# Kernel tuning notes

Hardware: AMD Instinct MI355X
Metric: run time of the kernel (lower is better)

The kernel has to match this reference:

```python
import jax, jax.numpy as jnp
import numpy as np
import math

EMB = 2048
HEADS = 16
HEAD_DIM = EMB // HEADS  # 128
SCALE = math.sqrt(HEAD_DIM)


def srms_norm(x, eps_min=1e-12):
    # Scaled RMS norm over last dim, computed in float32.
    d = x.shape[-1]
    xf = x.astype(jnp.float32)
    norm = jnp.linalg.norm(xf * (1.0 / math.sqrt(d)), axis=-1, keepdims=True)
    norm = jnp.maximum(norm, eps_min)
    return (xf / norm).astype(x.dtype)


def setup_inputs() -> dict:
    key = jax.random.key(0)
    ks = jax.random.split(key, 6)
    x = jax.random.normal(ks[0], (4, 4096, EMB), dtype=jnp.float32)
    # xavier-normal std for square D x D: sqrt(2/(D+D)) = 1/sqrt(D); gain=1 (lth=None)
    std = 1.0 / math.sqrt(EMB)
    Wq = jax.random.normal(ks[1], (EMB, EMB), dtype=jnp.float32) * std
    Wk = jax.random.normal(ks[2], (EMB, EMB), dtype=jnp.float32) * std
    Wv = jax.random.normal(ks[3], (EMB, EMB), dtype=jnp.float32) * std
    Wu = jax.random.normal(ks[4], (EMB, EMB), dtype=jnp.float32) * std
    Wo = jax.random.normal(ks[5], (EMB, EMB), dtype=jnp.float32) * std
    return {"x": x, "Wq": Wq, "Wk": Wk, "Wv": Wv, "Wu": Wu, "Wo": Wo}


def reference(x, Wq, Wk, Wv, Wu, Wo):
    B, L, D = x.shape
    H, dh = HEADS, HEAD_DIM
    # projections (weights stored as [in, out])
    q = (x @ Wq).reshape(B, L, H, dh).transpose(0, 2, 1, 3)  # [B,H,L,dh]
    k = (x @ Wk).reshape(B, L, H, dh).transpose(0, 2, 1, 3)
    v = (x @ Wv).reshape(B, L, H, dh).transpose(0, 2, 1, 3)
    u = (x @ Wu).reshape(B, L, H, dh).transpose(0, 2, 1, 3)
    q = jax.nn.relu(q) / SCALE
    k = jax.nn.relu(k) / SCALE
    u = jax.nn.silu(u)
    # linear retention: kv state [B,H,dh,dh], then q @ kv
    kv = jnp.einsum('bhlk,bhlv->bhkv', k, v)
    out = jnp.einsum('bhlk,bhkv->bhlv', q, kv)
    out = srms_norm(out) * u
    out = out.transpose(0, 2, 1, 3).reshape(B, L, D)
    return out @ Wo
```

## Files before the change

### kernel.cpp

```cpp
#include <hip/hip_runtime.h>
#include <hip/hip_bf16.h>
#include <cstdint>


typedef __attribute__((ext_vector_type(8))) short short8;
typedef __attribute__((ext_vector_type(4))) float f32x4;

#define DEVI static __device__ __forceinline__

DEVI float bf2f(unsigned short u) {
    union { unsigned int i; float f; } w; w.i = ((unsigned int)u) << 16; return w.f;
}
DEVI unsigned short f2bf(float f) {
    union { float f; unsigned int i; } w; w.f = f;
    return (unsigned short)((w.i + 0x7fffu + ((w.i >> 16) & 1u)) >> 16);
}

#define GLDS16(gp, lp) __builtin_amdgcn_global_load_lds( \
    (const __attribute__((address_space(1))) void*)(gp), \
    (__attribute__((address_space(3))) void*)(lp), 16, 0, 0)

__global__ void probe_dtype(const unsigned short* __restrict__ x, int* flag) {
    __shared__ int cnt;
    if (threadIdx.x == 0) cnt = 0;
    __syncthreads();
    int c = 0;
    for (int i = threadIdx.x; i < 4096; i += 256) {
        float a = fabsf(bf2f(x[i]));
        if (!(a <= 1e4f) || (a != 0.0f && a < 1e-4f)) ++c;
    }
    atomicAdd(&cnt, c);
    __syncthreads();
    if (threadIdx.x == 0) *flag = (cnt < 512) ? 1 : 0;
}

__global__ void wconvert(const void* __restrict__ Wq, const void* __restrict__ Wk,
                         const void* __restrict__ Wv, const void* __restrict__ Wu,
                         const void* __restrict__ Wo,
                         unsigned short* __restrict__ wt4,
                         unsigned short* __restrict__ wot,
                         const int* __restrict__ flag) {
    const int z = blockIdx.z;
    const void* W = (z == 0) ? Wq : (z == 1) ? Wk : (z == 2) ? Wv : (z == 3) ? Wu : Wo;
    const bool isbf = (*flag != 0);
    __shared__ float tile[32][33];
    const int j0 = blockIdx.x * 32, i0 = blockIdx.y * 32;
    const int tx = threadIdx.x, ty = threadIdx.y;
#pragma unroll
    for (int r = 0; r < 4; ++r) {
        const int i = i0 + ty * 4 + r;
        float v;
        if (isbf) v = bf2f(((const unsigned short*)W)[i * 2048 + j0 + tx]);
        else      v = ((const float*)W)[i * 2048 + j0 + tx];
        tile[ty * 4 + r][tx] = v;
    }
    __syncthreads();
#pragma unroll
    for (int r = 0; r < 4; ++r) {
        const int j = j0 + ty * 4 + r;
        const unsigned short bv = f2bf(tile[tx][ty * 4 + r]);
        if (z < 4) wt4[(long)(z * 2048 + j) * 2048 + i0 + tx] = bv;
        else       wot[(long)j * 2048 + i0 + tx] = bv;
    }
}

__global__ void xconvert(const void* __restrict__ X, unsigned short* __restrict__ xb,
                         const int* __restrict__ flag) {
    const bool isbf = (*flag != 0);
    const long i = (long)blockIdx.x * 256 + threadIdx.x;
    if (isbf) {
        ((uint4*)xb)[i] = ((const uint4*)X)[i];
    } else {
        const float4 f0 = ((const float4*)X)[2 * i];
        const float4 f1 = ((const float4*)X)[2 * i + 1];
        union { unsigned short us[8]; uint4 v; } o;
        o.us[0] = f2bf(f0.x); o.us[1] = f2bf(f0.y); o.us[2] = f2bf(f0.z); o.us[3] = f2bf(f0.w);
        o.us[4] = f2bf(f1.x); o.us[5] = f2bf(f1.y); o.us[6] = f2bf(f1.z); o.us[7] = f2bf(f1.w);
        ((uint4*)xb)[i] = o.v;
    }
}

DEVI void gemm_core(const unsigned short* __restrict__ Ag,
                    const unsigned short* __restrict__ Bg,
                    unsigned short* As, unsigned short* Bs,
                    f32x4 acc[8][4], const int tid) {
    const int wave = tid >> 6, lane = tid & 63;
    const int wr = wave >> 2, wc = wave & 3;
    const int srow = tid >> 2;
    const int lsl = (tid & 3) ^ ((srow >> 1) & 3);
    const unsigned short* ga0 = Ag + (long)srow * 2048 + lsl * 8;
    const unsigned short* ga1 = ga0 + 128 * 2048;
    const unsigned short* gb0 = Bg + (long)srow * 2048 + lsl * 8;
    const unsigned short* gb1 = gb0 + 128 * 2048;
    const int ldsb = wave * 512;

    const int psl = ((lane >> 4) ^ (((lane & 15) >> 1) & 3)) * 8;
    const int abase = (wr * 128 + (lane & 15)) * 32 + psl;
    const int bbase = (wc * 64 + (lane & 15)) * 32 + psl;

#define ISSUE(tt) do { \
    const int _b = (tt) & 3; const int _ko = (tt) * 32; \
    GLDS16(ga0 + _ko, As + _b * 8192 + ldsb); \
    GLDS16(ga1 + _ko, As + _b * 8192 + 4096 + ldsb); \
    GLDS16(gb0 + _ko, Bs + _b * 8192 + ldsb); \
    GLDS16(gb1 + _ko, Bs + _b * 8192 + 4096 + ldsb); \
} while (0)

    ISSUE(0); ISSUE(1); ISSUE(2);
    for (int t = 0; t < 64; ++t) {
        asm volatile("s_waitcnt vmcnt(8)" ::: "memory");
        asm volatile("s_barrier" ::: "memory");
        int tt = t + 3; if (tt >= 64) tt -= 64;
        ISSUE(tt);
        const unsigned short* a_ = As + (t & 3) * 8192;
        const unsigned short* b_ = Bs + (t & 3) * 8192;
        short8 af[8], bf[4];
#pragma unroll
        for (int fm = 0; fm < 8; ++fm) af[fm] = *(const short8*)(a_ + abase + fm * 512);
#pragma unroll
        for (int fn = 0; fn < 4; ++fn) bf[fn] = *(const short8*)(b_ + bbase + fn * 512);
        __builtin_amdgcn_s_setprio(1);
#pragma unroll
        for (int fm = 0; fm < 8; ++fm)
#pragma unroll
            for (int fn = 0; fn < 4; ++fn)
                acc[fm][fn] = __builtin_amdgcn_mfma_f32_16x16x32_bf16(af[fm], bf[fn], acc[fm][fn], 0, 0, 0);
        __builtin_amdgcn_s_setprio(0);
        asm volatile("s_barrier" ::: "memory");
    }
    asm volatile("s_waitcnt vmcnt(0)" ::: "memory");
#undef ISSUE
}

__global__ __launch_bounds__(512, 2)
void gemm_qkvu(const unsigned short* __restrict__ Xb,
               const unsigned short* __restrict__ Wt4,
               unsigned short* __restrict__ Qb, unsigned short* __restrict__ Kb,
               unsigned short* __restrict__ Vb, unsigned short* __restrict__ Ub) {
    __shared__ unsigned short As[4 * 8192];
    __shared__ unsigned short Bs[4 * 8192];
    const int orig = blockIdx.x;
    const int flat = (orig & 7) * 256 + (orig >> 3);
    const int mt = flat & 63, nt = flat >> 6;
    const long m0 = (long)mt * 256;
    const int tid = threadIdx.x;
    f32x4 acc[8][4] = {};

    gemm_core(Xb + m0 * 2048, Wt4 + (long)nt * 256 * 2048, As, Bs, acc, tid);

    const int wave = tid >> 6, lane = tid & 63;
    const int wr = wave >> 2, wc = wave & 3;
    const int seg = nt >> 3;
    unsigned short* outp = (seg == 0) ? Qb : (seg == 1) ? Kb : (seg == 2) ? Vb : Ub;
    const int cl0 = (nt & 7) * 256 + wc * 64;
#pragma unroll
    for (int fm = 0; fm < 8; ++fm) {
#pragma unroll
        for (int fn = 0; fn < 4; ++fn) {
            const int col = cl0 + fn * 16 + (lane & 15);
#pragma unroll
            for (int r = 0; r < 4; ++r) {
                const long row = m0 + wr * 128 + fm * 16 + ((lane >> 4) << 2) + r;
                float v = acc[fm][fn][r];
                if (seg <= 1)      v = fmaxf(v, 0.0f) * 0.08838834764831845f;
                else if (seg == 3) v = v / (1.0f + __expf(-v));
                outp[row * 2048 + col] = f2bf(v);
            }
        }
    }
}

__global__ __launch_bounds__(512, 2)
void gemm_out(const unsigned short* __restrict__ Obuf,
              const unsigned short* __restrict__ Wot,
              void* __restrict__ out, const int* __restrict__ flag) {
    __shared__ unsigned short As[4 * 8192];
    __shared__ unsigned short Bs[4 * 8192];
    const int orig = blockIdx.x;
    const int flat = (orig & 7) * 64 + (orig >> 3);
    const int mt = flat & 63, nt = flat >> 6;
    const long m0 = (long)mt * 256;
    const int j0 = nt * 256;
    const int tid = threadIdx.x;
    f32x4 acc[8][4] = {};

    gemm_core(Obuf + m0 * 2048, Wot + (long)j0 * 2048, As, Bs, acc, tid);

    const int wave = tid >> 6, lane = tid & 63;
    const int wr = wave >> 2, wc = wave & 3;
    const bool isbf = (*flag != 0);
#pragma unroll
    for (int fm = 0; fm < 8; ++fm) {
#pragma unroll
        for (int fn = 0; fn < 4; ++fn) {
            const int col = j0 + wc * 64 + fn * 16 + (lane & 15);
#pragma unroll
            for (int r = 0; r < 4; ++r) {
                const long row = m0 + wr * 128 + fm * 16 + ((lane >> 4) << 2) + r;
                const float v = acc[fm][fn][r];
                if (isbf) ((unsigned short*)out)[row * 2048 + col] = f2bf(v);
                else      ((float*)out)[row * 2048 + col] = v;
            }
        }
    }
}

__global__ void kv_accum(const unsigned short* __restrict__ Kb,
                         const unsigned short* __restrict__ Vb,
                         float* __restrict__ KVpart) {
    __shared__ unsigned short Kt[128 * 64];
    __shared__ unsigned short Vt[128 * 64];
    const int bh = blockIdx.x;
    const int chunk = blockIdx.y;
    const int b = bh >> 4, h = bh & 15;
    const int t = threadIdx.x, wave = t >> 6, lane = t & 63;
    const int wr = wave >> 1, wc = wave & 1;
    const int l0 = (t & 15) * 4;
    const int dkg = t >> 4;
    const long gbase = ((long)b * 4096 + chunk * 1024) * 2048 + h * 128;
    f32x4 acc[4][4] = {};

    for (int tile = 0; tile < 16; ++tile) {
        __syncthreads();
        short8 kr[4], vr[4];
#pragma unroll
        for (int li = 0; li < 4; ++li) {
            const long go = gbase + (long)(tile * 64 + l0 + li) * 2048 + dkg * 8;
            kr[li] = *(const short8*)(Kb + go);
            vr[li] = *(const short8*)(Vb + go);
        }
#pragma unroll
        for (int i = 0; i < 8; ++i) {
            const int row = dkg * 8 + i;
            const int lin = row * 128 + l0 * 2;
            const int off = (lin ^ ((row & 7) << 4)) >> 1;
            union { unsigned short us[4]; unsigned long long u; } pk, pv;
#pragma unroll
            for (int li = 0; li < 4; ++li) { pk.us[li] = (unsigned short)kr[li][i]; pv.us[li] = (unsigned short)vr[li][i]; }
            *(unsigned long long*)(Kt + off) = pk.u;
            *(unsigned long long*)(Vt + off) = pv.u;
        }
        __syncthreads();
#pragma unroll
        for (int ks = 0; ks < 2; ++ks) {
            const int kof = ks * 64 + (lane >> 4) * 16;
            short8 a[4], bfr[4];
#pragma unroll
            for (int f = 0; f < 4; ++f) {
                const int ra = wr * 64 + f * 16 + (lane & 15);
                const int rb = wc * 64 + f * 16 + (lane & 15);
                a[f]   = *(const short8*)(Vt + (((ra * 128 + kof) ^ ((ra & 7) << 4)) >> 1));
                bfr[f] = *(const short8*)(Kt + (((rb * 128 + kof) ^ ((rb & 7) << 4)) >> 1));
            }
#pragma unroll
            for (int fm = 0; fm < 4; ++fm)
#pragma unroll
                for (int fn = 0; fn < 4; ++fn)
                    acc[fm][fn] = __builtin_amdgcn_mfma_f32_16x16x32_bf16(a[fm], bfr[fn], acc[fm][fn], 0, 0, 0);
        }
    }
    float* dst = KVpart + ((long)chunk * 64 + bh) * 16384;
#pragma unroll
    for (int fm = 0; fm < 4; ++fm)
#pragma unroll
        for (int fn = 0; fn < 4; ++fn)
#pragma unroll
            for (int r = 0; r < 4; ++r) {
                const int dv = wr * 64 + fm * 16 + ((lane >> 4) << 2) + r;
                const int dk = wc * 64 + fn * 16 + (lane & 15);
                dst[dv * 128 + dk] = acc[fm][fn][r];
            }
}

__global__ void kv_finalize(const float* __restrict__ KVpart,
                            unsigned short* __restrict__ KVhi,
                            unsigned short* __restrict__ KVlo) {
    const long base = ((long)blockIdx.x * 256 + threadIdx.x) * 4;
    float4 s0 = *(const float4*)(KVpart + base);
    const float4 s1 = *(const float4*)(KVpart + 1048576 + base);
    const float4 s2 = *(const float4*)(KVpart + 2097152 + base);
    const float4 s3 = *(const float4*)(KVpart + 3145728 + base);
    float s[4] = { s0.x + s1.x + s2.x + s3.x, s0.y + s1.y + s2.y + s3.y,
                   s0.z + s1.z + s2.z + s3.z, s0.w + s1.w + s2.w + s3.w };
    union { unsigned short us[4]; unsigned long long u; } hi, lo;
#pragma unroll
    for (int j = 0; j < 4; ++j) {
        hi.us[j] = f2bf(s[j]);
        lo.us[j] = f2bf(s[j] - bf2f(hi.us[j]));
    }
    *(unsigned long long*)(KVhi + base) = hi.u;
    *(unsigned long long*)(KVlo + base) = lo.u;
}

__global__ void o_norm(const unsigned short* __restrict__ Qb,
                       const unsigned short* __restrict__ Ub,
                       const unsigned short* __restrict__ KVhi,
                       const unsigned short* __restrict__ KVlo,
                       unsigned short* __restrict__ Ob) {
    __shared__ unsigned short Qs[128 * 128];
    const int tid = threadIdx.x, wave = tid >> 6, lane = tid & 63;
    const int tile = blockIdx.x;
    const int bh = blockIdx.y;
    const int b = bh >> 4, h = bh & 15;
    const long n0 = (long)b * 4096 + tile * 128;

    const int qrow = tid >> 4;
    const int qcol = (tid & 15) * 8;
#pragma unroll
    for (int i = 0; i < 8; ++i)
        GLDS16(Qb + (n0 + i * 16 + qrow) * 2048 + h * 128 + qcol, Qs + i * 2048 + wave * 512);
    __syncthreads();

    const unsigned short* KH = KVhi + (long)bh * 16384;
    const unsigned short* KL = KVlo + (long)bh * 16384;
    f32x4 acc[2][8] = {};
#pragma unroll
    for (int kk = 0; kk < 4; ++kk) {
        const short8 a0 = *(const short8*)(Qs + (wave * 32 + (lane & 15)) * 128 + kk * 32 + (lane >> 4) * 8);
        const short8 a1 = *(const short8*)(Qs + (wave * 32 + 16 + (lane & 15)) * 128 + kk * 32 + (lane >> 4) * 8);
#pragma unroll
        for (int fn = 0; fn < 8; ++fn) {
            const int bo = (fn * 16 + (lane & 15)) * 128 + kk * 32 + (lane >> 4) * 8;
            const short8 bhi = *(const short8*)(KH + bo);
            const short8 blo = *(const short8*)(KL + bo);
            acc[0][fn] = __builtin_amdgcn_mfma_f32_16x16x32_bf16(a0, bhi, acc[0][fn], 0, 0, 0);
            acc[0][fn] = __builtin_amdgcn_mfma_f32_16x16x32_bf16(a0, blo, acc[0][fn], 0, 0, 0);
            acc[1][fn] = __builtin_amdgcn_mfma_f32_16x16x32_bf16(a1, bhi, acc[1][fn], 0, 0, 0);
            acc[1][fn] = __builtin_amdgcn_mfma_f32_16x16x32_bf16(a1, blo, acc[1][fn], 0, 0, 0);
        }
    }

#pragma unroll
    for (int fm = 0; fm < 2; ++fm) {
#pragma unroll
        for (int r = 0; r < 4; ++r) {
            float ssq = 0.0f;
#pragma unroll
            for (int fn = 0; fn < 8; ++fn) { const float v = acc[fm][fn][r]; ssq += v * v; }
            ssq += __shfl_xor(ssq, 1);
            ssq += __shfl_xor(ssq, 2);
            ssq += __shfl_xor(ssq, 4);
            ssq += __shfl_xor(ssq, 8);
            const float nrm = fmaxf(sqrtf(ssq) * 0.08838834764831845f, 1e-12f);
            const float scl = 1.0f / nrm;
            const long row = n0 + wave * 32 + fm * 16 + ((lane >> 4) << 2) + r;
#pragma unroll
            for (int fn = 0; fn < 8; ++fn) {
                const int col = fn * 16 + (lane & 15);
                const float uv = bf2f(Ub[row * 2048 + h * 128 + col]);
                Ob[row * 2048 + h * 128 + col] = f2bf(acc[fm][fn][r] * scl * uv);
            }
        }
    }
}

extern "C" void kernel_launch(void* const* d_in, const int* in_sizes, int n_in,
                              void* d_out, int out_size, void* d_ws, size_t ws_size,
                              hipStream_t stream) {
    (void)in_sizes; (void)n_in; (void)out_size; (void)ws_size;
    char* ws = (char*)d_ws;
    unsigned short* Xb  = (unsigned short*)(ws + 0);
    unsigned short* Wt4 = (unsigned short*)(ws + 67108864);
    unsigned short* Wot = (unsigned short*)(ws + 100663296);
    unsigned short* Qb  = (unsigned short*)(ws + 109051904);
    unsigned short* Kb  = (unsigned short*)(ws + 176160768);
    unsigned short* Vb  = (unsigned short*)(ws + 243269632);
    unsigned short* Ub  = (unsigned short*)(ws + 310378496);
    int*            flag= (int*)(ws + 381681664);
    float*          KVpart = (float*)Wt4;
    unsigned short* KVhi   = (unsigned short*)(ws + 67108864 + 16777216);
    unsigned short* KVlo   = (unsigned short*)(ws + 67108864 + 18874368);
    unsigned short* Ob     = Xb;

    probe_dtype<<<1, 256, 0, stream>>>((const unsigned short*)d_in[0], flag);
    wconvert<<<dim3(64, 64, 5), dim3(32, 8), 0, stream>>>(d_in[1], d_in[2], d_in[3],
                                                          d_in[4], d_in[5], Wt4, Wot, flag);
    xconvert<<<16384, 256, 0, stream>>>(d_in[0], Xb, flag);
    gemm_qkvu<<<2048, 512, 0, stream>>>(Xb, Wt4, Qb, Kb, Vb, Ub);
    kv_accum<<<dim3(64, 4), 256, 0, stream>>>(Kb, Vb, KVpart);
    kv_finalize<<<1024, 256, 0, stream>>>(KVpart, KVhi, KVlo);
    o_norm<<<dim3(32, 64), 256, 0, stream>>>(Qb, Ub, KVhi, KVlo, Ob);
    gemm_out<<<512, 512, 0, stream>>>(Ob, Wot, d_out, flag);
}
```

Measured before the change: 1.195 ms.

## Split GEMM k-step into two phases interleaving LDS reads, global loads, and MFMAs

Restructures the GEMM main loop into two half-phases. Each phase loads part of the A/B fragments from LDS, issues half of the next tile's global-to-LDS loads, synchronizes with barriers, then runs half of the MFMAs. The aim is to overlap memory traffic with matrix math and reduce register pressure from holding all fragments at once, in the style of ping-pong scheduling. In exchange it adds barriers per iteration, which may cost synchronization overhead.

```diff
diff --git a/kernel.cpp b/kernel.cpp
--- a/kernel.cpp
+++ b/kernel.cpp
@@ -98,38 +98,55 @@
     const int abase = (wr * 128 + (lane & 15)) * 32 + psl;
     const int bbase = (wc * 64 + (lane & 15)) * 32 + psl;
 
-#define ISSUE(tt) do { \
-    const int _b = (tt) & 3; const int _ko = (tt) * 32; \
+#define ISA(tt) do { const int _b = (tt) & 3; const int _ko = (tt) * 32; \
     GLDS16(ga0 + _ko, As + _b * 8192 + ldsb); \
-    GLDS16(ga1 + _ko, As + _b * 8192 + 4096 + ldsb); \
+    GLDS16(ga1 + _ko, As + _b * 8192 + 4096 + ldsb); } while (0)
+#define ISB(tt) do { const int _b = (tt) & 3; const int _ko = (tt) * 32; \
     GLDS16(gb0 + _ko, Bs + _b * 8192 + ldsb); \
-    GLDS16(gb1 + _ko, Bs + _b * 8192 + 4096 + ldsb); \
-} while (0)
-
-    ISSUE(0); ISSUE(1); ISSUE(2);
+    GLDS16(gb1 + _ko, Bs + _b * 8192 + 4096 + ldsb); } while (0)
+
+    ISA(0); ISB(0); ISA(1); ISB(1); ISA(2); ISB(2);
     for (int t = 0; t < 64; ++t) {
         asm volatile("s_waitcnt vmcnt(8)" ::: "memory");
-        asm volatile("s_barrier" ::: "memory");
-        int tt = t + 3; if (tt >= 64) tt -= 64;
-        ISSUE(tt);
+        __builtin_amdgcn_s_barrier();
         const unsigned short* a_ = As + (t & 3) * 8192;
         const unsigned short* b_ = Bs + (t & 3) * 8192;
-        short8 af[8], bf[4];
-#pragma unroll
-        for (int fm = 0; fm < 8; ++fm) af[fm] = *(const short8*)(a_ + abase + fm * 512);
-#pragma unroll
-        for (int fn = 0; fn < 4; ++fn) bf[fn] = *(const short8*)(b_ + bbase + fn * 512);
+        int tt = t + 3; if (tt >= 64) tt -= 64;
+
+        short8 a0[4], b0[4];
+#pragma unroll
+        for (int fm = 0; fm < 4; ++fm) a0[fm] = *(const short8*)(a_ + abase + fm * 512);
+#pragma unroll
+        for (int fn = 0; fn < 4; ++fn) b0[fn] = *(const short8*)(b_ + bbase + fn * 512);
+        ISA(tt);
+        __builtin_amdgcn_s_barrier();
+        asm volatile("s_waitcnt lgkmcnt(0)" ::: "memory");
         __builtin_amdgcn_s_setprio(1);
 #pragma unroll
-        for (int fm = 0; fm < 8; ++fm)
+        for (int fm = 0; fm < 4; ++fm)
 #pragma unroll
             for (int fn = 0; fn < 4; ++fn)
-                acc[fm][fn] = __builtin_amdgcn_mfma_f32_16x16x32_bf16(af[fm], bf[fn], acc[fm][fn], 0, 0, 0);
+                acc[fm][fn] = __builtin_amdgcn_mfma_f32_16x16x32_bf16(a0[fm], b0[fn], acc[fm][fn], 0, 0, 0);
         __builtin_amdgcn_s_setprio(0);
-        asm volatile("s_barrier" ::: "memory");
+        __builtin_amdgcn_s_barrier();
+
+        short8 a1[4];
+#pragma unroll
+        for (int fm = 0; fm < 4; ++fm) a1[fm] = *(const short8*)(a_ + abase + (4 + fm) * 512);
+        ISB(tt);
+        __builtin_amdgcn_s_barrier();
+        asm volatile("s_waitcnt lgkmcnt(0)" ::: "memory");
+        __builtin_amdgcn_s_setprio(1);
+#pragma unroll
+        for (int fm = 0; fm < 4; ++fm)
+#pragma unroll
+            for (int fn = 0; fn < 4; ++fn)
+                acc[4 + fm][fn] = __builtin_amdgcn_mfma_f32_16x16x32_bf16(a1[fm], b0[fn], acc[4 + fm][fn], 0, 0, 0);
+        __builtin_amdgcn_s_setprio(0);
     }
     asm volatile("s_waitcnt vmcnt(0)" ::: "memory");
-#undef ISSUE
+#undef ISA
+#undef ISB
 }
 
 __global__ __launch_bounds__(512, 2)
```

Result: slower. 1.242 ms (+3.9%).

## Double-buffer MFMA fragments in registers and deepen LDS prefetch to four stages

Applied to the files above, without the earlier changes.

Restructures the shared GEMM main loop so each k-step's LDS fragment reads are issued before the previous step's MFMA block runs, using two register fragment sets that alternate. The global-to-LDS prefetch grows from three stages to four, and the loop drops to one barrier per k-step, with explicit vmcnt and lgkmcnt waits. The aim is to hide LDS read latency and barrier stalls behind matrix-core work. The cost is a second set of fragment registers, which may cause spills or lower occupancy under the 512x2 launch bounds, plus more delicate wait-count reasoning.

```diff
diff --git a/kernel.cpp b/kernel.cpp
--- a/kernel.cpp
+++ b/kernel.cpp
@@ -98,38 +98,48 @@
     const int abase = (wr * 128 + (lane & 15)) * 32 + psl;
     const int bbase = (wc * 64 + (lane & 15)) * 32 + psl;
 
-#define ISSUE(tt) do { \
-    const int _b = (tt) & 3; const int _ko = (tt) * 32; \
+#define ISSUE(tt) do { const int _b = (tt) & 3; const int _ko = (tt) * 32; \
     GLDS16(ga0 + _ko, As + _b * 8192 + ldsb); \
     GLDS16(ga1 + _ko, As + _b * 8192 + 4096 + ldsb); \
     GLDS16(gb0 + _ko, Bs + _b * 8192 + ldsb); \
-    GLDS16(gb1 + _ko, Bs + _b * 8192 + 4096 + ldsb); \
-} while (0)
-
-    ISSUE(0); ISSUE(1); ISSUE(2);
-    for (int t = 0; t < 64; ++t) {
+    GLDS16(gb1 + _ko, Bs + _b * 8192 + 4096 + ldsb); } while (0)
+#define RDFRAG(aX, bX, buf) do { \
+    const unsigned short* _a = As + (buf) * 8192; \
+    const unsigned short* _b = Bs + (buf) * 8192; \
+    _Pragma("unroll") for (int fm = 0; fm < 8; ++fm) aX[fm] = *(const short8*)(_a + abase + fm * 512); \
+    _Pragma("unroll") for (int fn = 0; fn < 4; ++fn) bX[fn] = *(const short8*)(_b + bbase + fn * 512); } while (0)
+#define MFMACL(aX, bX) do { \
+    __builtin_amdgcn_s_setprio(1); \
+    _Pragma("unroll") for (int fm = 0; fm < 8; ++fm) \
+    _Pragma("unroll") for (int fn = 0; fn < 4; ++fn) \
+        acc[fm][fn] = __builtin_amdgcn_mfma_f32_16x16x32_bf16(aX[fm], bX[fn], acc[fm][fn], 0, 0, 0); \
+    __builtin_amdgcn_s_setprio(0); } while (0)
+
+    ISSUE(0); ISSUE(1); ISSUE(2); ISSUE(3);
+    asm volatile("s_waitcnt vmcnt(12)" ::: "memory");
+    asm volatile("s_barrier" ::: "memory");
+    short8 aE[8], bE[4], aO[8], bO[4];
+    RDFRAG(aE, bE, 0);
+
+    for (int tp = 0; tp < 32; ++tp) {
+        const int t = 2 * tp;
         asm volatile("s_waitcnt vmcnt(8)" ::: "memory");
         asm volatile("s_barrier" ::: "memory");
-        int tt = t + 3; if (tt >= 64) tt -= 64;
-        ISSUE(tt);
-        const unsigned short* a_ = As + (t & 3) * 8192;
-        const unsigned short* b_ = Bs + (t & 3) * 8192;
-        short8 af[8], bf[4];
-#pragma unroll
-        for (int fm = 0; fm < 8; ++fm) af[fm] = *(const short8*)(a_ + abase + fm * 512);
-#pragma unroll
-        for (int fn = 0; fn < 4; ++fn) bf[fn] = *(const short8*)(b_ + bbase + fn * 512);
-        __builtin_amdgcn_s_setprio(1);
-#pragma unroll
-        for (int fm = 0; fm < 8; ++fm)
-#pragma unroll
-            for (int fn = 0; fn < 4; ++fn)
-                acc[fm][fn] = __builtin_amdgcn_mfma_f32_16x16x32_bf16(af[fm], bf[fn], acc[fm][fn], 0, 0, 0);
-        __builtin_amdgcn_s_setprio(0);
+        RDFRAG(aO, bO, (t + 1) & 3);
+        asm volatile("s_waitcnt lgkmcnt(12)" ::: "memory");
+        { int ti = t + 4; if (ti >= 64) ti -= 64; ISSUE(ti); }
+        MFMACL(aE, bE);
+        asm volatile("s_waitcnt vmcnt(8)" ::: "memory");
         asm volatile("s_barrier" ::: "memory");
-    }
-    asm volatile("s_waitcnt vmcnt(0)" ::: "memory");
+        { int tr = t + 2; if (tr > 63) tr = 63; RDFRAG(aE, bE, tr & 3); }
+        asm volatile("s_waitcnt lgkmcnt(12)" ::: "memory");
+        { int ti = t + 5; if (ti >= 64) ti -= 64; ISSUE(ti); }
+        MFMACL(aO, bO);
+    }
+    asm volatile("s_waitcnt vmcnt(0) lgkmcnt(0)" ::: "memory");
 #undef ISSUE
+#undef RDFRAG
+#undef MFMACL
 }
 
 __global__ __launch_bounds__(512, 2)
```

New measurement: 987.5 us. 1.21x faster.
